# Kernel tuning notes

Hardware: AMD Instinct MI355X
Metric: run time of the kernel (lower is better)

## Reference

```python
import jax, jax.numpy as jnp
import numpy as np

SOFTMAX_SCALE = 1.0  # module default

def setup_inputs() -> dict:
    key = jax.random.key(0)
    ks = jax.random.split(key, 5)
    B, H, S, D = 2, 8, 192, 64
    shp = (B, H, S, D)
    return {
        "q":  jax.random.normal(ks[0], shp, dtype=jnp.float32),
        "k1": jax.random.normal(ks[1], shp, dtype=jnp.float32),
        "k2": jax.random.normal(ks[2], shp, dtype=jnp.float32),
        "v1": jax.random.normal(ks[3], shp, dtype=jnp.float32),
        "v2": jax.random.normal(ks[4], shp, dtype=jnp.float32),
    }

def reference(q, k1, k2, v1, v2):
    B, H, S, D = q.shape
    # trilinear scores: torch einsum 'bnth,bnsh,bnqh->bntsq' then rearrange to [b,n,q,(t s)]
    # equivalently compute [b,n,q,t,s] directly
    scores = jnp.einsum('bnth,bnsh,bnqh->bnqts', k1, k2, q)  # [B,H,S,S,S]
    flat = scores.reshape(B, H, S, S * S) * SOFTMAX_SCALE
    m = jnp.max(flat, axis=-1, keepdims=True)               # [B,H,S,1]
    p = jnp.exp(flat - m)
    suma = jnp.sum(p, axis=-1, keepdims=True)
    attn = (p / suma).reshape(B, H, S, S, S)                # [B,H,q,t,s]
    z = jnp.einsum('bnqts,bntd->bnqd', attn, v1) + jnp.einsum('bnqts,bnsd->bnqd', attn, v2)
    lse = m[..., 0] + jnp.log(suma[..., 0])                 # [B,H,S]
    return (z, lse)
```

## Files before the change

kernel.cpp:

```cpp
#include <hip/hip_runtime.h>
#include <hip/hip_bf16.h>
#include <math.h>


#define SS 192
#define DD 64
#define NT 512

typedef __attribute__((ext_vector_type(8))) short bf16x8;
typedef __attribute__((ext_vector_type(4))) float f32x4;

static __device__ __forceinline__ unsigned pk_bf16(float a, float b) {
    union { __hip_bfloat162 h; unsigned u; } cv;
    cv.h = __float22bfloat162_rn(float2{a, b});
    return cv.u;
}

#define DPP_STEP(v, CTRL)                                                   \
    (v) += __int_as_float(__builtin_amdgcn_update_dpp(                      \
        0, __float_as_int(v), (CTRL), 0xF, 0xF, true))

static __device__ __forceinline__ float row16_sum(float v) {
    DPP_STEP(v, 0xB1);
    DPP_STEP(v, 0x4E);
    DPP_STEP(v, 0x141);
    DPP_STEP(v, 0x140);
    return v;
}

__global__ __launch_bounds__(256) void k2_pack(const float* __restrict__ k2g,
                                               uint4* __restrict__ outp) {
    int i = blockIdx.x * 256 + threadIdx.x;
    const float4* in = (const float4*)k2g;
    float4 a = in[2 * i], b = in[2 * i + 1];
    uint4 w;
    w.x = pk_bf16(a.x, a.y);
    w.y = pk_bf16(a.z, a.w);
    w.z = pk_bf16(b.x, b.y);
    w.w = pk_bf16(b.z, b.w);
    int ih = i & 1535;
    int r = ih >> 3, c = ih & 7;
    outp[(i & ~1535) | (r * 8 + (c ^ (r & 7)))] = w;
}

__launch_bounds__(NT, 4)
__global__ void tritt_fwd(const float* __restrict__ qg,
                          const float* __restrict__ k1g,
                          const uint4* __restrict__ k2p,
                          const float* __restrict__ v1g,
                          const float* __restrict__ v2g,
                          float* __restrict__ zg,
                          float* __restrict__ lseg) {
    __shared__ uint4 wl[SS * 8];
    __shared__ uint4 k2l[SS * 8];
    __shared__ float At[SS];
    __shared__ float As[SS];
    __shared__ float zsh[DD];

    const int tid = threadIdx.x;
    const int bid = blockIdx.x;
    const int head = bid / SS;
    const size_t hb = (size_t)head * SS * DD;

    const uint4* k2h = k2p + (size_t)head * (SS * 8);
    #pragma unroll
    for (int it = 0; it < (SS * 8) / NT; ++it) {
        int f8 = tid + it * NT;
        __builtin_amdgcn_global_load_lds(
            (const __attribute__((address_space(1))) unsigned int*)(k2h + f8),
            (__attribute__((address_space(3))) unsigned int*)&k2l[f8],
            16, 0, 0);
    }

    if (tid < SS) At[tid] = 0.f;
    else if (tid < 2 * SS) As[tid - SS] = 0.f;
    else if (tid < 2 * SS + DD) zsh[tid - 2 * SS] = 0.f;

    const float L2E = 1.44269504088896340736f;
    const float4* k1v = (const float4*)(k1g + hb);
    const float4* qv  = (const float4*)(qg + (size_t)bid * DD);
    {
        const int c = tid & 7;
        float4 q0 = qv[2 * c], q1 = qv[2 * c + 1];
        q0.x *= L2E; q0.y *= L2E; q0.z *= L2E; q0.w *= L2E;
        q1.x *= L2E; q1.y *= L2E; q1.z *= L2E; q1.w *= L2E;
        #pragma unroll 1
        for (int it = 0; it < (SS * 8) / NT; ++it) {
            int f8 = tid + it * NT;
            int r = f8 >> 3;
            float4 a0 = k1v[2 * f8], a1 = k1v[2 * f8 + 1];
            uint4 w;
            w.x = pk_bf16(a0.x * q0.x, a0.y * q0.y);
            w.y = pk_bf16(a0.z * q0.z, a0.w * q0.w);
            w.z = pk_bf16(a1.x * q1.x, a1.y * q1.y);
            w.w = pk_bf16(a1.z * q1.z, a1.w * q1.w);
            wl[r * 8 + (c ^ (r & 7))] = w;
        }
    }
    __syncthreads();

    const int lane = tid & 63;
    const int wid  = tid >> 6;
    const int wt   = wid >> 2;
    const int ws   = wid & 3;
    const int lrow = lane & 15;
    const int lk   = lane >> 4;
    const int lrm  = lrow & 7;

    const int sw0 = lk ^ lrm;
    const int sw1 = (4 + lk) ^ lrm;
    const int ab  = (wt * 96 + lrow) * 8;
    const int bb  = (ws * 48 + lrow) * 8;

    float colp[3] = {0.f, 0.f, 0.f};
    #pragma unroll
    for (int i = 0; i < 6; ++i) {
        f32x4 acc[3];
        #pragma unroll
        for (int j = 0; j < 3; ++j) acc[j] = (f32x4){0.f, 0.f, 0.f, 0.f};
        {
            bf16x8 afr = *(const bf16x8*)&wl[ab + i * 128 + sw0];
            #pragma unroll
            for (int j = 0; j < 3; ++j) {
                bf16x8 bfr = *(const bf16x8*)&k2l[bb + j * 128 + sw0];
                acc[j] = __builtin_amdgcn_mfma_f32_16x16x32_bf16(
                    afr, bfr, acc[j], 0, 0, 0);
            }
        }
        {
            bf16x8 afr = *(const bf16x8*)&wl[ab + i * 128 + sw1];
            #pragma unroll
            for (int j = 0; j < 3; ++j) {
                bf16x8 bfr = *(const bf16x8*)&k2l[bb + j * 128 + sw1];
                acc[j] = __builtin_amdgcn_mfma_f32_16x16x32_bf16(
                    afr, bfr, acc[j], 0, 0, 0);
            }
        }
        float rs[4] = {0.f, 0.f, 0.f, 0.f};
        #pragma unroll
        for (int j = 0; j < 3; ++j)
            #pragma unroll
            for (int r = 0; r < 4; ++r) {
                float p = __builtin_amdgcn_exp2f(acc[j][r]);
                rs[r] += p;
                colp[j] += p;
            }
        #pragma unroll
        for (int r = 0; r < 4; ++r) {
            float v = row16_sum(rs[r]);
            if (lrow == 0)
                atomicAdd(&At[wt * 96 + i * 16 + lk * 4 + r], v);
        }
    }
    #pragma unroll
    for (int j = 0; j < 3; ++j) {
        float v = colp[j];
        v += __shfl_xor(v, 16, 64);
        v += __shfl_xor(v, 32, 64);
        if (lane < 16)
            atomicAdd(&As[ws * 48 + j * 16 + lane], v);
    }
    __syncthreads();

    float suma = At[lane] + At[lane + 64] + At[lane + 128];
    suma = row16_sum(suma);
    suma += __shfl_xor(suma, 16, 64);
    suma += __shfl_xor(suma, 32, 64);

    const int d = tid & 63;
    const int g = tid >> 6;
    const float* v1p = v1g + hb;
    const float* v2p = v2g + hb;
    float zp = 0.f;
    #pragma unroll 4
    for (int r = 0; r < 24; ++r) {
        int t = g * 24 + r;
        zp = fmaf(At[t], v1p[t * DD + d], zp);
        zp = fmaf(As[t], v2p[t * DD + d], zp);
    }
    atomicAdd(&zsh[d], zp);
    __syncthreads();

    if (tid < DD) zg[(size_t)bid * DD + tid] = zsh[tid] / suma;
    if (tid == 0) lseg[bid] = logf(suma);
}

extern "C" void kernel_launch(void* const* d_in, const int* in_sizes, int n_in,
                              void* d_out, int out_size, void* d_ws, size_t ws_size,
                              hipStream_t stream) {
    const float* q  = (const float*)d_in[0];
    const float* k1 = (const float*)d_in[1];
    const float* k2 = (const float*)d_in[2];
    const float* v1 = (const float*)d_in[3];
    const float* v2 = (const float*)d_in[4];
    float* out = (float*)d_out;

    const int nq = in_sizes[0] / DD;
    const int nheads = nq / SS;
    float* zout   = out;
    float* lseout = out + (size_t)nq * DD;
    uint4* k2pack = (uint4*)d_ws;

    int n8 = nheads * SS * DD / 8;
    hipLaunchKernelGGL(k2_pack, dim3(n8 / 256), dim3(256), 0, stream, k2, k2pack);

    dim3 grid(nq), block(NT);
    hipLaunchKernelGGL(tritt_fwd, grid, block, 0, stream,
                       q, k1, (const uint4*)k2pack, v1, v2, zout, lseout);
}
```

Measured before the change: 59.89 us.

## Process two query rows per block to reuse K2 staging and V loads

Each block now handles two consecutive query rows instead of one, halving the grid. The k2 tile loaded into LDS, the k1 reads and the v1/v2 reads in the output stage are shared across both queries, which cuts per-query global traffic and block setup overhead. In exchange LDS use rises with a second weighted-k1 buffer and larger reduction arrays, which may lower occupancy. Only 1536 blocks remain for the whole GPU, and the serial work per block doubles.

```diff
diff --git a/kernel.cpp b/kernel.cpp
--- a/kernel.cpp
+++ b/kernel.cpp
@@ -43,6 +43,10 @@
     outp[(i & ~1535) | (r * 8 + (c ^ (r & 7)))] = w;
 }
 
+#define AT(qq, t) red[(qq) * SS + (t)]
+#define AS(qq, s) red[2 * SS + (qq) * SS + (s)]
+#define ZSH(qq, d) red[4 * SS + (qq) * DD + (d)]
+
 __launch_bounds__(NT, 4)
 __global__ void tritt_fwd(const float* __restrict__ qg,
                           const float* __restrict__ k1g,
@@ -51,15 +55,13 @@
                           const float* __restrict__ v2g,
                           float* __restrict__ zg,
                           float* __restrict__ lseg) {
-    __shared__ uint4 wl[SS * 8];
     __shared__ uint4 k2l[SS * 8];
-    __shared__ float At[SS];
-    __shared__ float As[SS];
-    __shared__ float zsh[DD];
+    __shared__ uint4 wl[2][SS * 8];
+    __shared__ float red[4 * SS + 2 * DD];
 
     const int tid = threadIdx.x;
-    const int bid = blockIdx.x;
-    const int head = bid / SS;
+    const int q0 = 2 * blockIdx.x;
+    const int head = q0 / SS;
     const size_t hb = (size_t)head * SS * DD;
 
     const uint4* k2h = k2p + (size_t)head * (SS * 8);
@@ -72,29 +74,37 @@
             16, 0, 0);
     }
 
-    if (tid < SS) At[tid] = 0.f;
-    else if (tid < 2 * SS) As[tid - SS] = 0.f;
-    else if (tid < 2 * SS + DD) zsh[tid - 2 * SS] = 0.f;
+    red[tid] = 0.f;
+    if (tid < 4 * SS + 2 * DD - NT) red[tid + NT] = 0.f;
 
     const float L2E = 1.44269504088896340736f;
     const float4* k1v = (const float4*)(k1g + hb);
-    const float4* qv  = (const float4*)(qg + (size_t)bid * DD);
+    const float4* qv0 = (const float4*)(qg + (size_t)q0 * DD);
     {
         const int c = tid & 7;
-        float4 q0 = qv[2 * c], q1 = qv[2 * c + 1];
-        q0.x *= L2E; q0.y *= L2E; q0.z *= L2E; q0.w *= L2E;
-        q1.x *= L2E; q1.y *= L2E; q1.z *= L2E; q1.w *= L2E;
+        float4 p00 = qv0[2 * c], p01 = qv0[2 * c + 1];
+        float4 p10 = qv0[16 + 2 * c], p11 = qv0[16 + 2 * c + 1];
+        p00.x *= L2E; p00.y *= L2E; p00.z *= L2E; p00.w *= L2E;
+        p01.x *= L2E; p01.y *= L2E; p01.z *= L2E; p01.w *= L2E;
+        p10.x *= L2E; p10.y *= L2E; p10.z *= L2E; p10.w *= L2E;
+        p11.x *= L2E; p11.y *= L2E; p11.z *= L2E; p11.w *= L2E;
         #pragma unroll 1
         for (int it = 0; it < (SS * 8) / NT; ++it) {
             int f8 = tid + it * NT;
             int r = f8 >> 3;
+            int idx = r * 8 + (c ^ (r & 7));
             float4 a0 = k1v[2 * f8], a1 = k1v[2 * f8 + 1];
             uint4 w;
-            w.x = pk_bf16(a0.x * q0.x, a0.y * q0.y);
-            w.y = pk_bf16(a0.z * q0.z, a0.w * q0.w);
-            w.z = pk_bf16(a1.x * q1.x, a1.y * q1.y);
-            w.w = pk_bf16(a1.z * q1.z, a1.w * q1.w);
-            wl[r * 8 + (c ^ (r & 7))] = w;
+            w.x = pk_bf16(a0.x * p00.x, a0.y * p00.y);
+            w.y = pk_bf16(a0.z * p00.z, a0.w * p00.w);
+            w.z = pk_bf16(a1.x * p01.x, a1.y * p01.y);
+            w.w = pk_bf16(a1.z * p01.z, a1.w * p01.w);
+            wl[0][idx] = w;
+            w.x = pk_bf16(a0.x * p10.x, a0.y * p10.y);
+            w.y = pk_bf16(a0.z * p10.z, a0.w * p10.w);
+            w.z = pk_bf16(a1.x * p11.x, a1.y * p11.y);
+            w.w = pk_bf16(a1.z * p11.z, a1.w * p11.w);
+            wl[1][idx] = w;
         }
     }
     __syncthreads();
@@ -112,77 +122,93 @@
     const int ab  = (wt * 96 + lrow) * 8;
     const int bb  = (ws * 48 + lrow) * 8;
 
-    float colp[3] = {0.f, 0.f, 0.f};
     #pragma unroll
-    for (int i = 0; i < 6; ++i) {
-        f32x4 acc[3];
+    for (int qq = 0; qq < 2; ++qq) {
+        const uint4* wlq = wl[qq];
+        float colp[3] = {0.f, 0.f, 0.f};
         #pragma unroll
-        for (int j = 0; j < 3; ++j) acc[j] = (f32x4){0.f, 0.f, 0.f, 0.f};
-        {
-            bf16x8 afr = *(const bf16x8*)&wl[ab + i * 128 + sw0];
+        for (int i = 0; i < 6; ++i) {
+            f32x4 acc[3];
             #pragma unroll
-            for (int j = 0; j < 3; ++j) {
-                bf16x8 bfr = *(const bf16x8*)&k2l[bb + j * 128 + sw0];
-                acc[j] = __builtin_amdgcn_mfma_f32_16x16x32_bf16(
-                    afr, bfr, acc[j], 0, 0, 0);
+            for (int j = 0; j < 3; ++j) acc[j] = (f32x4){0.f, 0.f, 0.f, 0.f};
+            {
+                bf16x8 afr = *(const bf16x8*)&wlq[ab + i * 128 + sw0];
+                #pragma unroll
+                for (int j = 0; j < 3; ++j) {
+                    bf16x8 bfr = *(const bf16x8*)&k2l[bb + j * 128 + sw0];
+                    acc[j] = __builtin_amdgcn_mfma_f32_16x16x32_bf16(
+                        afr, bfr, acc[j], 0, 0, 0);
+                }
+            }
+            {
+                bf16x8 afr = *(const bf16x8*)&wlq[ab + i * 128 + sw1];
+                #pragma unroll
+                for (int j = 0; j < 3; ++j) {
+                    bf16x8 bfr = *(const bf16x8*)&k2l[bb + j * 128 + sw1];
+                    acc[j] = __builtin_amdgcn_mfma_f32_16x16x32_bf16(
+                        afr, bfr, acc[j], 0, 0, 0);
+                }
+            }
+            float rs[4] = {0.f, 0.f, 0.f, 0.f};
+            #pragma unroll
+            for (int j = 0; j < 3; ++j)
+                #pragma unroll
+                for (int r = 0; r < 4; ++r) {
+                    float p = __builtin_amdgcn_exp2f(acc[j][r]);
+                    rs[r] += p;
+                    colp[j] += p;
+                }
+            #pragma unroll
+            for (int r = 0; r < 4; ++r) {
+                float v = row16_sum(rs[r]);
+                if (lrow == 0)
+                    atomicAdd(&AT(qq, wt * 96 + i * 16 + lk * 4 + r), v);
             }
         }
-        {
-            bf16x8 afr = *(const bf16x8*)&wl[ab + i * 128 + sw1];
-            #pragma unroll
-            for (int j = 0; j < 3; ++j) {
-                bf16x8 bfr = *(const bf16x8*)&k2l[bb + j * 128 + sw1];
-                acc[j] = __builtin_amdgcn_mfma_f32_16x16x32_bf16(
-                    afr, bfr, acc[j], 0, 0, 0);
-            }
+        #pragma unroll
+        for (int j = 0; j < 3; ++j) {
+            float v = colp[j];
+            v += __shfl_xor(v, 16, 64);
+            v += __shfl_xor(v, 32, 64);
+            if (lane < 16)
+                atomicAdd(&AS(qq, ws * 48 + j * 16 + lane), v);
         }
-        float rs[4] = {0.f, 0.f, 0.f, 0.f};
-        #pragma unroll
-        for (int j = 0; j < 3; ++j)
-            #pragma unroll
-            for (int r = 0; r < 4; ++r) {
-                float p = __builtin_amdgcn_exp2f(acc[j][r]);
-                rs[r] += p;
-                colp[j] += p;
-            }
-        #pragma unroll
-        for (int r = 0; r < 4; ++r) {
-            float v = row16_sum(rs[r]);
-            if (lrow == 0)
-                atomicAdd(&At[wt * 96 + i * 16 + lk * 4 + r], v);
-        }
-    }
-    #pragma unroll
-    for (int j = 0; j < 3; ++j) {
-        float v = colp[j];
-        v += __shfl_xor(v, 16, 64);
-        v += __shfl_xor(v, 32, 64);
-        if (lane < 16)
-            atomicAdd(&As[ws * 48 + j * 16 + lane], v);
     }
     __syncthreads();
 
-    float suma = At[lane] + At[lane + 64] + At[lane + 128];
-    suma = row16_sum(suma);
-    suma += __shfl_xor(suma, 16, 64);
-    suma += __shfl_xor(suma, 32, 64);
+    float suma0 = AT(0, lane) + AT(0, lane + 64) + AT(0, lane + 128);
+    suma0 = row16_sum(suma0);
+    suma0 += __shfl_xor(suma0, 16, 64);
+    suma0 += __shfl_xor(suma0, 32, 64);
+    float suma1 = AT(1, lane) + AT(1, lane + 64) + AT(1, lane + 128);
+    suma1 = row16_sum(suma1);
+    suma1 += __shfl_xor(suma1, 16, 64);
+    suma1 += __shfl_xor(suma1, 32, 64);
 
     const int d = tid & 63;
     const int g = tid >> 6;
     const float* v1p = v1g + hb;
     const float* v2p = v2g + hb;
-    float zp = 0.f;
+    float zp0 = 0.f, zp1 = 0.f;
     #pragma unroll 4
     for (int r = 0; r < 24; ++r) {
         int t = g * 24 + r;
-        zp = fmaf(At[t], v1p[t * DD + d], zp);
-        zp = fmaf(As[t], v2p[t * DD + d], zp);
-    }
-    atomicAdd(&zsh[d], zp);
+        float x1 = v1p[t * DD + d];
+        float x2 = v2p[t * DD + d];
+        zp0 = fmaf(AT(0, t), x1, fmaf(AS(0, t), x2, zp0));
+        zp1 = fmaf(AT(1, t), x1, fmaf(AS(1, t), x2, zp1));
+    }
+    atomicAdd(&ZSH(0, d), zp0);
+    atomicAdd(&ZSH(1, d), zp1);
     __syncthreads();
 
-    if (tid < DD) zg[(size_t)bid * DD + tid] = zsh[tid] / suma;
-    if (tid == 0) lseg[bid] = logf(suma);
+    if (tid < DD) {
+        zg[(size_t)q0 * DD + tid] = ZSH(0, tid) / suma0;
+    } else if (tid < 2 * DD) {
+        zg[(size_t)(q0 + 1) * DD + (tid - DD)] = ZSH(1, tid - DD) / suma1;
+    }
+    if (tid == 0) lseg[q0] = logf(suma0);
+    if (tid == 1) lseg[q0 + 1] = logf(suma1);
 }
 
 extern "C" void kernel_launch(void* const* d_in, const int* in_sizes, int n_in,
@@ -204,7 +230,7 @@
     int n8 = nheads * SS * DD / 8;
     hipLaunchKernelGGL(k2_pack, dim3(n8 / 256), dim3(256), 0, stream, k2, k2pack);
 
-    dim3 grid(nq), block(NT);
+    dim3 grid(nq / 2), block(NT);
     hipLaunchKernelGGL(tritt_fwd, grid, block, 0, stream,
                        q, k1, (const uint4*)k2pack, v1, v2, zout, lseout);
 }
```

Result: faster. 54.28 us, median of 2 (-9.4%).

## Split each query's t-range across two blocks and combine partials in a finish kernel

Applied to the files above, without the earlier changes.

Each query row's work over the t dimension is divided between two blocks, each covering 96 t rows against all 192 s columns. Partial z vectors and softmax sums are written to workspace, and a new small kernel adds them, normalizes, and writes z and lse. The aim is to double the grid size for better CU occupancy and latency hiding, at the cost of an extra launch, a redundant k2 LDS load per block, and a round trip through global memory for the partials. The max-free exp2 softmax from before is kept.

```diff
diff --git a/kernel.cpp b/kernel.cpp
--- a/kernel.cpp
+++ b/kernel.cpp
@@ -4,6 +4,7 @@
 
 
 #define SS 192
+#define TH 96
 #define DD 64
 #define NT 512
 
@@ -44,22 +45,21 @@
 }
 
 __launch_bounds__(NT, 4)
-__global__ void tritt_fwd(const float* __restrict__ qg,
-                          const float* __restrict__ k1g,
-                          const uint4* __restrict__ k2p,
-                          const float* __restrict__ v1g,
-                          const float* __restrict__ v2g,
-                          float* __restrict__ zg,
-                          float* __restrict__ lseg) {
-    __shared__ uint4 wl[SS * 8];
+__global__ void tritt_half(const float* __restrict__ qg,
+                           const float* __restrict__ k1g,
+                           const uint4* __restrict__ k2p,
+                           const float* __restrict__ v1g,
+                           const float* __restrict__ v2g,
+                           float* __restrict__ partial) {
     __shared__ uint4 k2l[SS * 8];
-    __shared__ float At[SS];
-    __shared__ float As[SS];
-    __shared__ float zsh[DD];
+    __shared__ uint4 wl[TH * 8];
+    __shared__ float red[TH + SS + DD];
 
     const int tid = threadIdx.x;
     const int bid = blockIdx.x;
-    const int head = bid / SS;
+    const int q   = bid >> 1;
+    const int th  = bid & 1;
+    const int head = q / SS;
     const size_t hb = (size_t)head * SS * DD;
 
     const uint4* k2h = k2p + (size_t)head * (SS * 8);
@@ -72,29 +72,31 @@
             16, 0, 0);
     }
 
-    if (tid < SS) At[tid] = 0.f;
-    else if (tid < 2 * SS) As[tid - SS] = 0.f;
-    else if (tid < 2 * SS + DD) zsh[tid - 2 * SS] = 0.f;
+    if (tid < TH + SS + DD) red[tid] = 0.f;
 
     const float L2E = 1.44269504088896340736f;
     const float4* k1v = (const float4*)(k1g + hb);
-    const float4* qv  = (const float4*)(qg + (size_t)bid * DD);
+    const float4* qv  = (const float4*)(qg + (size_t)q * DD);
     {
         const int c = tid & 7;
-        float4 q0 = qv[2 * c], q1 = qv[2 * c + 1];
-        q0.x *= L2E; q0.y *= L2E; q0.z *= L2E; q0.w *= L2E;
-        q1.x *= L2E; q1.y *= L2E; q1.z *= L2E; q1.w *= L2E;
+        float4 p0 = qv[2 * c], p1 = qv[2 * c + 1];
+        p0.x *= L2E; p0.y *= L2E; p0.z *= L2E; p0.w *= L2E;
+        p1.x *= L2E; p1.y *= L2E; p1.z *= L2E; p1.w *= L2E;
         #pragma unroll 1
-        for (int it = 0; it < (SS * 8) / NT; ++it) {
+        for (int it = 0; it < 2; ++it) {
             int f8 = tid + it * NT;
-            int r = f8 >> 3;
-            float4 a0 = k1v[2 * f8], a1 = k1v[2 * f8 + 1];
-            uint4 w;
-            w.x = pk_bf16(a0.x * q0.x, a0.y * q0.y);
-            w.y = pk_bf16(a0.z * q0.z, a0.w * q0.w);
-            w.z = pk_bf16(a1.x * q1.x, a1.y * q1.y);
-            w.w = pk_bf16(a1.z * q1.z, a1.w * q1.w);
-            wl[r * 8 + (c ^ (r & 7))] = w;
+            if (f8 < TH * 8) {
+                int r = f8 >> 3;
+                int gt = th * TH + r;
+                float4 a0 = k1v[gt * 16 + 2 * c];
+                float4 a1 = k1v[gt * 16 + 2 * c + 1];
+                uint4 w;
+                w.x = pk_bf16(a0.x * p0.x, a0.y * p0.y);
+                w.y = pk_bf16(a0.z * p0.z, a0.w * p0.w);
+                w.z = pk_bf16(a1.x * p1.x, a1.y * p1.y);
+                w.w = pk_bf16(a1.z * p1.z, a1.w * p1.w);
+                wl[r * 8 + (c ^ (r & 7))] = w;
+            }
         }
     }
     __syncthreads();
@@ -102,54 +104,40 @@
     const int lane = tid & 63;
     const int wid  = tid >> 6;
     const int wt   = wid >> 2;
-    const int ws   = wid & 3;
+    const int ws4  = wid & 3;
     const int lrow = lane & 15;
     const int lk   = lane >> 4;
     const int lrm  = lrow & 7;
-
     const int sw0 = lk ^ lrm;
     const int sw1 = (4 + lk) ^ lrm;
-    const int ab  = (wt * 96 + lrow) * 8;
-    const int bb  = (ws * 48 + lrow) * 8;
+    const int ab  = (wt * 48 + lrow) * 8;
+    const int bb  = (ws4 * 48 + lrow) * 8;
 
     float colp[3] = {0.f, 0.f, 0.f};
     #pragma unroll
-    for (int i = 0; i < 6; ++i) {
-        f32x4 acc[3];
-        #pragma unroll
-        for (int j = 0; j < 3; ++j) acc[j] = (f32x4){0.f, 0.f, 0.f, 0.f};
-        {
-            bf16x8 afr = *(const bf16x8*)&wl[ab + i * 128 + sw0];
-            #pragma unroll
-            for (int j = 0; j < 3; ++j) {
-                bf16x8 bfr = *(const bf16x8*)&k2l[bb + j * 128 + sw0];
-                acc[j] = __builtin_amdgcn_mfma_f32_16x16x32_bf16(
-                    afr, bfr, acc[j], 0, 0, 0);
-            }
-        }
-        {
-            bf16x8 afr = *(const bf16x8*)&wl[ab + i * 128 + sw1];
-            #pragma unroll
-            for (int j = 0; j < 3; ++j) {
-                bf16x8 bfr = *(const bf16x8*)&k2l[bb + j * 128 + sw1];
-                acc[j] = __builtin_amdgcn_mfma_f32_16x16x32_bf16(
-                    afr, bfr, acc[j], 0, 0, 0);
-            }
-        }
+    for (int i = 0; i < 3; ++i) {
+        bf16x8 afr0 = *(const bf16x8*)&wl[ab + i * 128 + sw0];
+        bf16x8 afr1 = *(const bf16x8*)&wl[ab + i * 128 + sw1];
         float rs[4] = {0.f, 0.f, 0.f, 0.f};
         #pragma unroll
-        for (int j = 0; j < 3; ++j)
+        for (int j = 0; j < 3; ++j) {
+            f32x4 acc = (f32x4){0.f, 0.f, 0.f, 0.f};
+            bf16x8 b0 = *(const bf16x8*)&k2l[bb + j * 128 + sw0];
+            acc = __builtin_amdgcn_mfma_f32_16x16x32_bf16(afr0, b0, acc, 0, 0, 0);
+            bf16x8 b1 = *(const bf16x8*)&k2l[bb + j * 128 + sw1];
+            acc = __builtin_amdgcn_mfma_f32_16x16x32_bf16(afr1, b1, acc, 0, 0, 0);
             #pragma unroll
             for (int r = 0; r < 4; ++r) {
-                float p = __builtin_amdgcn_exp2f(acc[j][r]);
+                float p = __builtin_amdgcn_exp2f(acc[r]);
                 rs[r] += p;
                 colp[j] += p;
             }
+        }
         #pragma unroll
         for (int r = 0; r < 4; ++r) {
             float v = row16_sum(rs[r]);
             if (lrow == 0)
-                atomicAdd(&At[wt * 96 + i * 16 + lk * 4 + r], v);
+                atomicAdd(&red[wt * 48 + i * 16 + lk * 4 + r], v);
         }
     }
     #pragma unroll
@@ -158,31 +146,52 @@
         v += __shfl_xor(v, 16, 64);
         v += __shfl_xor(v, 32, 64);
         if (lane < 16)
-            atomicAdd(&As[ws * 48 + j * 16 + lane], v);
+            atomicAdd(&red[TH + ws4 * 48 + j * 16 + lane], v);
     }
     __syncthreads();
 
-    float suma = At[lane] + At[lane + 64] + At[lane + 128];
-    suma = row16_sum(suma);
-    suma += __shfl_xor(suma, 16, 64);
-    suma += __shfl_xor(suma, 32, 64);
-
-    const int d = tid & 63;
-    const int g = tid >> 6;
+    float suma = 0.f;
+    if (wid == 0) {
+        float s = red[lane] + ((lane < 32) ? red[64 + lane] : 0.f);
+        #pragma unroll
+        for (int off = 1; off < 64; off <<= 1)
+            s += __shfl_xor(s, off, 64);
+        suma = s;
+    }
+
+    const int d = lane;
+    const int g = wid;
     const float* v1p = v1g + hb;
     const float* v2p = v2g + hb;
     float zp = 0.f;
     #pragma unroll 4
+    for (int r = 0; r < 12; ++r) {
+        int tl = g * 12 + r;
+        zp = fmaf(red[tl], v1p[(size_t)(th * TH + tl) * DD + d], zp);
+    }
+    #pragma unroll 4
     for (int r = 0; r < 24; ++r) {
-        int t = g * 24 + r;
-        zp = fmaf(At[t], v1p[t * DD + d], zp);
-        zp = fmaf(As[t], v2p[t * DD + d], zp);
-    }
-    atomicAdd(&zsh[d], zp);
+        int s = g * 24 + r;
+        zp = fmaf(red[TH + s], v2p[(size_t)s * DD + d], zp);
+    }
+    atomicAdd(&red[TH + SS + d], zp);
     __syncthreads();
 
-    if (tid < DD) zg[(size_t)bid * DD + tid] = zsh[tid] / suma;
-    if (tid == 0) lseg[bid] = logf(suma);
+    float* slot = partial + ((size_t)q * 2 + th) * 72;
+    if (tid < DD) slot[tid] = red[TH + SS + tid];
+    if (tid == 0) slot[64] = suma;
+}
+
+__global__ __launch_bounds__(256) void tritt_fin(const float* __restrict__ partial,
+                                                 float* __restrict__ zg,
+                                                 float* __restrict__ lseg) {
+    int idx = blockIdx.x * 256 + threadIdx.x;
+    int q = idx >> 6, d = idx & 63;
+    const float* s0 = partial + (size_t)q * 144;
+    const float* s1 = s0 + 72;
+    float suma = s0[64] + s1[64];
+    zg[(size_t)q * DD + d] = (s0[d] + s1[d]) / suma;
+    if (d == 0) lseg[q] = logf(suma);
 }
 
 extern "C" void kernel_launch(void* const* d_in, const int* in_sizes, int n_in,
@@ -199,12 +208,16 @@
     const int nheads = nq / SS;
     float* zout   = out;
     float* lseout = out + (size_t)nq * DD;
-    uint4* k2pack = (uint4*)d_ws;
+
+    uint4* k2pack  = (uint4*)d_ws;
+    float* partial = (float*)((char*)d_ws + (size_t)nheads * SS * 8 * 16);
 
     int n8 = nheads * SS * DD / 8;
     hipLaunchKernelGGL(k2_pack, dim3(n8 / 256), dim3(256), 0, stream, k2, k2pack);
 
-    dim3 grid(nq), block(NT);
-    hipLaunchKernelGGL(tritt_fwd, grid, block, 0, stream,
-                       q, k1, (const uint4*)k2pack, v1, v2, zout, lseout);
-}
+    hipLaunchKernelGGL(tritt_half, dim3(nq * 2), dim3(NT), 0, stream,
+                       q, k1, (const uint4*)k2pack, v1, v2, partial);
+
+    hipLaunchKernelGGL(tritt_fin, dim3(nq * DD / 256), dim3(256), 0, stream,
+                       partial, zout, lseout);
+}
```

Result: slower. 77.42 us (+29.3%).
